# Performance work log

Hardware: AMD Instinct MI355X
Metric: run time of the kernel (lower is better)

Reference implementation:

```python
import jax, jax.numpy as jnp
import numpy as np

B, T, D, P, C = 65536, 3, 512, 32, 10  # batch, views, x_dim, p_dim, num_classes

def setup_inputs() -> dict:
    key = jax.random.key(0)
    ks = jax.random.split(key, 6)
    return {
        "x": jax.random.normal(ks[0], (B, T, D), dtype=jnp.float32),
        "Wk": jax.random.normal(ks[1], (P, D), dtype=jnp.float32) * (1.0 / np.sqrt(D)),
        "Wv": jax.random.normal(ks[2], (P, D), dtype=jnp.float32) * (1.0 / np.sqrt(D)),
        "Wq": jax.random.normal(ks[3], (P, T * D), dtype=jnp.float32) * (1.0 / np.sqrt(T * D)),
        "Wfc": jax.random.normal(ks[4], (C, P), dtype=jnp.float32) * (1.0 / np.sqrt(P)),
        "bfc": jax.random.normal(ks[5], (C,), dtype=jnp.float32) * 0.01,
    }

def reference(x, Wk, Wv, Wq, Wfc, bfc):
    # x: [B, 3, D]. Per-sample: k_i = Wk x_i, v_i = Wv x_i, q = Wq concat(x1,x2,x3)
    k = jnp.einsum('btd,pd->btp', x, Wk)                 # [B,3,P]
    v = jnp.einsum('btd,pd->btp', x, Wv)                 # [B,3,P]
    q = jnp.einsum('bf,pf->bp', x.reshape(x.shape[0], -1), Wq)  # [B,P]
    a = jax.nn.softmax(jnp.einsum('bp,btp->bt', q, k), axis=-1)  # 3-way softmax [B,3]
    c = jnp.einsum('bt,btp->bp', a, v)                   # weighted sum [B,P]
    return c @ Wfc.T + bfc                               # [B,C]
```

## Files before the change

kernel.cpp:

```cpp
#include <hip/hip_runtime.h>


typedef __attribute__((ext_vector_type(4))) float  f32x4;
typedef __attribute__((ext_vector_type(8))) _Float16 h16x8;

#define T_VIEWS 3
#define D_DIM   512
#define P_DIM   32
#define C_DIM   10
#define NROWS   80
#define NT      5
#define KC      16
#define NSTEPS  48
#define JPER    4
#define NSUPER  (NSTEPS/JPER)
#define STEP_B  (NT*1024)
#define CHUNK_B (JPER*STEP_B)
#define WAVES_PER_BLOCK 4
#define SAMPLES_PER_BLOCK (16 * WAVES_PER_BLOCK)

__global__ void build_weights(const float* __restrict__ Wk,
                              const float* __restrict__ Wv,
                              const float* __restrict__ Wq,
                              const float* __restrict__ Wfc,
                              _Float16* __restrict__ Wf) {
    const int row = blockIdx.x;
    const int t   = row / NROWS;
    const int j   = row % NROWS;
    const int d   = threadIdx.x;
    float val;
    if (j < 32) {
        val = Wk[j * D_DIM + d];
    } else if (j < 64) {
        const int p = j - 32;
        val = Wq[p * (T_VIEWS * D_DIM) + t * D_DIM + d];
    } else if (j < 64 + C_DIM) {
        const int i = j - 64;
        float s = 0.f;
        #pragma unroll
        for (int p = 0; p < P_DIM; ++p)
            s += Wfc[i * P_DIM + p] * Wv[p * D_DIM + d];
        val = s;
    } else {
        val = 0.f;
    }
    const int n = j >> 4, coln = j & 15;
    const int kc = d >> 5, r = d & 31;
    const int quad = (r >> 2) & 3;
    const int jj   = ((r >> 4) << 2) | (r & 3);
    const size_t addr = (size_t)((((t * KC + kc) * NT + n) * 64) + quad * 16 + coln) * 8 + jj;
    Wf[addr] = (_Float16)val;
}

__global__ __launch_bounds__(256, 4) void attn_fused(
        const float* __restrict__ x,
        const _Float16* __restrict__ Wf,
        const float* __restrict__ bfc,
        float* __restrict__ out) {
    __shared__ char lds[2 * CHUNK_B];

    const int lane = threadIdx.x & 63;
    const int wave = threadIdx.x >> 6;
    const int col  = lane & 15;
    const int quad = lane >> 4;
    const int row_base = blockIdx.x * SAMPLES_PER_BLOCK + wave * 16;

    f32x4 acc_k[3][2];
    f32x4 acc_q[2];
    f32x4 acc_y[3];
    #pragma unroll
    for (int t = 0; t < 3; ++t) {
        acc_k[t][0] = (f32x4)0.f;
        acc_k[t][1] = (f32x4)0.f;
        acc_y[t]    = (f32x4)0.f;
    }
    acc_q[0] = (f32x4)0.f;
    acc_q[1] = (f32x4)0.f;

    const float* xbase = x + (size_t)(row_base + col) * (T_VIEWS * D_DIM) + quad * 4;
    const char*  wf   = (const char*)Wf + lane * 16;

    #pragma unroll
    for (int i = 0; i < 5; ++i) {
        const int idx = wave * 5 + i;
        __builtin_amdgcn_global_load_lds(
            (const __attribute__((address_space(1))) void*)(wf + (size_t)idx * 1024),
            (__attribute__((address_space(3))) void*)(lds + idx * 1024),
            16, 0, 0);
    }
    __syncthreads();

    for (int u = 0; u < NSUPER; ++u) {
        const int cbuf = u & 1;
        const int nbuf = cbuf ^ 1;
        if (u + 1 < NSUPER) {
            #pragma unroll
            for (int i = 0; i < 5; ++i) {
                const int idx = wave * 5 + i;
                const size_t gb = (size_t)(u + 1) * CHUNK_B + (size_t)idx * 1024;
                __builtin_amdgcn_global_load_lds(
                    (const __attribute__((address_space(1))) void*)(wf + gb),
                    (__attribute__((address_space(3))) void*)(lds + nbuf * CHUNK_B + idx * 1024),
                    16, 0, 0);
            }
        }
        #pragma unroll
        for (int j = 0; j < JPER; ++j) {
            const int s  = u * JPER + j;
            const int t  = s >> 4;
            const int kc = s & 15;
            const float* xp = xbase + t * D_DIM + kc * 32;
            const f32x4 x0 = __builtin_nontemporal_load((const f32x4*)xp);
            const f32x4 x1 = __builtin_nontemporal_load((const f32x4*)(xp + 16));
            h16x8 b[NT];
            #pragma unroll
            for (int n = 0; n < NT; ++n)
                b[n] = *(const h16x8*)(lds + cbuf * CHUNK_B + j * STEP_B + n * 1024 + lane * 16);
            h16x8 a;
            #pragma unroll
            for (int i = 0; i < 4; ++i) {
                a[i]     = (_Float16)x0[i];
                a[i + 4] = (_Float16)x1[i];
            }
            acc_k[t][0] = __builtin_amdgcn_mfma_f32_16x16x32_f16(a, b[0], acc_k[t][0], 0, 0, 0);
            acc_k[t][1] = __builtin_amdgcn_mfma_f32_16x16x32_f16(a, b[1], acc_k[t][1], 0, 0, 0);
            acc_q[0]    = __builtin_amdgcn_mfma_f32_16x16x32_f16(a, b[2], acc_q[0],    0, 0, 0);
            acc_q[1]    = __builtin_amdgcn_mfma_f32_16x16x32_f16(a, b[3], acc_q[1],    0, 0, 0);
            acc_y[t]    = __builtin_amdgcn_mfma_f32_16x16x32_f16(a, b[4], acc_y[t],    0, 0, 0);
        }
        __syncthreads();
    }

    const float bias = (col < C_DIM) ? bfc[col] : 0.f;

    float outv[4];
    #pragma unroll
    for (int r = 0; r < 4; ++r) {
        const float qa = acc_q[0][r];
        const float qb = acc_q[1][r];
        float s0 = qa * acc_k[0][0][r] + qb * acc_k[0][1][r];
        float s1 = qa * acc_k[1][0][r] + qb * acc_k[1][1][r];
        float s2 = qa * acc_k[2][0][r] + qb * acc_k[2][1][r];
        #pragma unroll
        for (int msk = 1; msk <= 8; msk <<= 1) {
            s0 += __shfl_xor(s0, msk, 64);
            s1 += __shfl_xor(s1, msk, 64);
            s2 += __shfl_xor(s2, msk, 64);
        }
        const float mx = fmaxf(s0, fmaxf(s1, s2));
        const float e0 = __expf(s0 - mx);
        const float e1 = __expf(s1 - mx);
        const float e2 = __expf(s2 - mx);
        const float inv = 1.f / (e0 + e1 + e2);
        outv[r] = (e0 * acc_y[0][r] + e1 * acc_y[1][r] + e2 * acc_y[2][r]) * inv + bias;
    }
    if (col < C_DIM) {
        const int b0 = row_base + quad * 4;
        #pragma unroll
        for (int r = 0; r < 4; ++r)
            out[(size_t)(b0 + r) * C_DIM + col] = outv[r];
    }
}

extern "C" void kernel_launch(void* const* d_in, const int* in_sizes, int n_in,
                              void* d_out, int out_size, void* d_ws, size_t ws_size,
                              hipStream_t stream) {
    const float* x   = (const float*)d_in[0];
    const float* Wk  = (const float*)d_in[1];
    const float* Wv  = (const float*)d_in[2];
    const float* Wq  = (const float*)d_in[3];
    const float* Wfc = (const float*)d_in[4];
    const float* bfc = (const float*)d_in[5];
    _Float16* Wf = (_Float16*)d_ws;

    hipLaunchKernelGGL(build_weights, dim3(T_VIEWS * NROWS), dim3(D_DIM), 0, stream,
                       Wk, Wv, Wq, Wfc, Wf);

    const int B_TOTAL = in_sizes[0] / (T_VIEWS * D_DIM);
    const int blocks = B_TOTAL / SAMPLES_PER_BLOCK;
    hipLaunchKernelGGL(attn_fused, dim3(blocks), dim3(256), 0, stream,
                       x, Wf, bfc, (float*)d_out);
}
```

Measured before the change: 533.2 us.

## Software-pipeline x loads two stages ahead with explicit vmcnt waits

Fully unrolls the super-step loop and keeps activation loads in two register buffers, issuing loads for step u+2 while computing step u. The default barrier is replaced by manual s_waitcnt vmcnt plus s_barrier, so outstanding x loads do not block progress while weight LDS prefetches finish. This hides global load latency behind MFMA work. The cost is more registers (launch bounds lowered to 3 blocks per SM), lower occupancy, and fragile hand-counted vmcnt values.

```diff
diff --git a/kernel.cpp b/kernel.cpp
--- a/kernel.cpp
+++ b/kernel.cpp
@@ -52,7 +52,7 @@
     Wf[addr] = (_Float16)val;
 }
 
-__global__ __launch_bounds__(256, 4) void attn_fused(
+__global__ __launch_bounds__(256, 3) void attn_fused(
         const float* __restrict__ x,
         const _Float16* __restrict__ Wf,
         const float* __restrict__ bfc,
@@ -78,49 +78,44 @@
     acc_q[1] = (f32x4)0.f;
 
     const float* xbase = x + (size_t)(row_base + col) * (T_VIEWS * D_DIM) + quad * 4;
-    const char*  wf   = (const char*)Wf + lane * 16;
-
-    #pragma unroll
-    for (int i = 0; i < 5; ++i) {
-        const int idx = wave * 5 + i;
-        __builtin_amdgcn_global_load_lds(
-            (const __attribute__((address_space(1))) void*)(wf + (size_t)idx * 1024),
-            (__attribute__((address_space(3))) void*)(lds + idx * 1024),
-            16, 0, 0);
-    }
-    __syncthreads();
-
-    for (int u = 0; u < NSUPER; ++u) {
-        const int cbuf = u & 1;
-        const int nbuf = cbuf ^ 1;
-        if (u + 1 < NSUPER) {
-            #pragma unroll
-            for (int i = 0; i < 5; ++i) {
-                const int idx = wave * 5 + i;
-                const size_t gb = (size_t)(u + 1) * CHUNK_B + (size_t)idx * 1024;
-                __builtin_amdgcn_global_load_lds(
-                    (const __attribute__((address_space(1))) void*)(wf + gb),
-                    (__attribute__((address_space(3))) void*)(lds + nbuf * CHUNK_B + idx * 1024),
-                    16, 0, 0);
-            }
-        }
+    const char*  wfg   = (const char*)Wf + lane * 16;
+
+    f32x4 xA[2 * JPER];
+    f32x4 xB[2 * JPER];
+
+    auto GLDS = [&](int u) {
+        #pragma unroll
+        for (int i = 0; i < 5; ++i) {
+            const int idx = wave * 5 + i;
+            __builtin_amdgcn_global_load_lds(
+                (const __attribute__((address_space(1))) void*)(wfg + (size_t)u * CHUNK_B + idx * 1024),
+                (__attribute__((address_space(3))) void*)(lds + (u & 1) * CHUNK_B + idx * 1024),
+                16, 0, 0);
+        }
+    };
+    auto LOADX = [&](int u, f32x4* xr) {
         #pragma unroll
         for (int j = 0; j < JPER; ++j) {
-            const int s  = u * JPER + j;
-            const int t  = s >> 4;
-            const int kc = s & 15;
+            const int s = u * JPER + j, t = s >> 4, kc = s & 15;
             const float* xp = xbase + t * D_DIM + kc * 32;
-            const f32x4 x0 = __builtin_nontemporal_load((const f32x4*)xp);
-            const f32x4 x1 = __builtin_nontemporal_load((const f32x4*)(xp + 16));
+            xr[2 * j]     = __builtin_nontemporal_load((const f32x4*)xp);
+            xr[2 * j + 1] = __builtin_nontemporal_load((const f32x4*)(xp + 16));
+        }
+    };
+    auto BODY = [&](int u, const f32x4* xr) {
+        const char* buf = lds + (u & 1) * CHUNK_B;
+        #pragma unroll
+        for (int j = 0; j < JPER; ++j) {
+            const int s = u * JPER + j, t = s >> 4;
             h16x8 b[NT];
             #pragma unroll
             for (int n = 0; n < NT; ++n)
-                b[n] = *(const h16x8*)(lds + cbuf * CHUNK_B + j * STEP_B + n * 1024 + lane * 16);
+                b[n] = *(const h16x8*)(buf + j * STEP_B + n * 1024 + lane * 16);
             h16x8 a;
             #pragma unroll
             for (int i = 0; i < 4; ++i) {
-                a[i]     = (_Float16)x0[i];
-                a[i + 4] = (_Float16)x1[i];
+                a[i]     = (_Float16)xr[2 * j][i];
+                a[i + 4] = (_Float16)xr[2 * j + 1][i];
             }
             acc_k[t][0] = __builtin_amdgcn_mfma_f32_16x16x32_f16(a, b[0], acc_k[t][0], 0, 0, 0);
             acc_k[t][1] = __builtin_amdgcn_mfma_f32_16x16x32_f16(a, b[1], acc_k[t][1], 0, 0, 0);
@@ -128,7 +123,30 @@
             acc_q[1]    = __builtin_amdgcn_mfma_f32_16x16x32_f16(a, b[3], acc_q[1],    0, 0, 0);
             acc_y[t]    = __builtin_amdgcn_mfma_f32_16x16x32_f16(a, b[4], acc_y[t],    0, 0, 0);
         }
-        __syncthreads();
+    };
+
+    GLDS(0);
+    LOADX(0, xA);
+    LOADX(1, xB);
+    asm volatile("s_waitcnt vmcnt(16)" ::: "memory");
+    __builtin_amdgcn_sched_barrier(0);
+    __builtin_amdgcn_s_barrier();
+
+    #pragma unroll
+    for (int u = 0; u < NSUPER; ++u) {
+        f32x4* xcur = (u & 1) ? xB : xA;
+        if (u + 1 < NSUPER) GLDS(u + 1);
+        BODY(u, xcur);
+        if (u + 2 < NSUPER) LOADX(u + 2, xcur);
+        if (u + 1 < NSUPER) {
+            if (u + 2 < NSUPER) {
+                asm volatile("s_waitcnt vmcnt(8)" ::: "memory");
+            } else {
+                asm volatile("s_waitcnt vmcnt(0)" ::: "memory");
+            }
+            __builtin_amdgcn_sched_barrier(0);
+            __builtin_amdgcn_s_barrier();
+        }
     }
 
     const float bias = (col < C_DIM) ? bfc[col] : 0.f;
```

New measurement: 524.7 us, median of 2. No clear change (-1.6%).
